# Kernel optimization log

Measured on AMD Instinct MI355X. Metric: run time of the kernel, lower is better.

## Reference

```python
import jax, jax.numpy as jnp
import numpy as np

NUM_RBF = 16
TOP_K = 30
MAXREL = 32  # max_relative_feature
M_CTX = 16   # ligand context atoms per residue

PT_GROUP = jnp.array([0,1,18,1,2,13,14,15,16,17,18,1,2,13,14,15,16,17,18,1,2,3,4,5,6,7,8,9,10,11,12,13,14,15,16,17,18,1,2,3,4,5,6,7,8,9,10,11,12,13,14,15,16,17,18,1,2,3,3,3,3,3,3,3,3,3,3,3,3,3,3,3,4,5,6,7,8,9,10,11,12,13,14,15,16,17,18,1,2,3,3,3,3,3,3,3,3,3,3,3,3,3,3,3,4,5,6,7,8,9,10,11,12,13,14,15,16,17,18], dtype=jnp.int32)
PT_PERIOD = jnp.array([0,1,1,2,2,2,2,2,2,2,2,3,3,3,3,3,3,3,3,4,4,4,4,4,4,4,4,4,4,4,4,4,4,4,4,4,4,5,5,5,5,5,5,5,5,5,5,5,5,5,5,5,5,5,5,6,6,6,6,6,6,6,6,6,6,6,6,6,6,6,6,6,6,6,6,6,6,6,6,6,6,6,6,6,6,6,6,7,7,7,7,7,7,7,7,7,7,7,7,7,7,7,7,7,7,7,7,7,7,7,7,7,7,7,7,7,7,7,7], dtype=jnp.int32)

# pair order after the Ca-Ca term: (N,N),(C,C),(O,O),(Cb,Cb),(Ca,N),(Ca,C),(Ca,O),(Ca,Cb),
# (N,C),(N,O),(N,Cb),(Cb,C),(Cb,O),(O,C),(N,Ca),(C,Ca),(O,Ca),(Cb,Ca),(C,N),(O,N),(Cb,N),(C,Cb),(O,Cb),(C,O)
# atom index in A5 stack: N=0, Ca=1, C=2, O=3, Cb=4
AI = np.array([0,2,3,4,1,1,1,1,0,0,0,4,4,3,0,2,3,4,2,3,4,2,3,2])
BI = np.array([0,2,3,4,0,2,3,4,2,3,4,2,3,2,1,1,1,1,0,0,0,4,4,3])


def _rbf(D):
    mu = jnp.linspace(2.0, 22.0, NUM_RBF)
    sigma = (22.0 - 2.0) / NUM_RBF
    return jnp.exp(-(((D[..., None] - mu) / sigma) ** 2))


def _angle_features(A, Bc, Cc, Y):
    v1 = A - Bc
    v2 = Cc - Bc
    e1 = v1 / jnp.linalg.norm(v1, axis=-1, keepdims=True)
    dot = jnp.einsum('bli,bli->bl', e1, v2)[..., None]
    u2 = v2 - e1 * dot
    e2 = u2 / jnp.linalg.norm(u2, axis=-1, keepdims=True)
    e3 = jnp.cross(e1, e2, axis=-1)
    R = jnp.concatenate((e1[..., None], e2[..., None], e3[..., None]), axis=-1)  # [B,L,3,3]
    lv = jnp.einsum('blqp,blyq->blyp', R, Y - Bc[:, :, None, :])
    rxy = jnp.sqrt(lv[..., 0] ** 2 + lv[..., 1] ** 2 + 1e-8)
    f1 = lv[..., 0] / rxy
    f2 = lv[..., 1] / rxy
    rxyz = jnp.linalg.norm(lv, axis=-1) + 1e-8
    f3 = rxy / rxyz
    f4 = lv[..., 2] / rxyz
    return jnp.stack([f1, f2, f3, f4], axis=-1)  # [B,L,M,4]


def setup_inputs() -> dict:
    key = jax.random.key(0)
    ks = jax.random.split(key, 16)
    B, L, M = 2, 2048, M_CTX
    X = jax.random.normal(ks[0], (B, L, 4, 3), jnp.float32) * 10.0
    Y = jax.random.normal(ks[1], (B, L, M, 3), jnp.float32) * 10.0
    mask = jnp.ones((B, L), jnp.float32)
    Y_m = jnp.ones((B, L, M), jnp.float32)
    R_idx = jnp.arange(B * L, dtype=jnp.int32).reshape(B, L)
    chain_labels = jax.random.randint(ks[2], (B, L), 0, 2, jnp.int32)
    Y_t = jax.random.randint(ks[3], (B, L, M), 1, 119, jnp.int32)
    def lin(k, fi, fo):
        return jax.random.normal(k, (fi, fo), jnp.float32) / np.sqrt(fi)
    params = dict(
        Wp=lin(ks[4], 2 * MAXREL + 2, 16), bp=jnp.zeros((16,), jnp.float32),
        We=lin(ks[5], 16 + 25 * NUM_RBF, 128), be=jnp.zeros((128,), jnp.float32),
        Wn=lin(ks[6], 5 * NUM_RBF + 64 + 4, 128), bn=jnp.zeros((128,), jnp.float32),
        Wt=lin(ks[7], 147, 64), bt=jnp.zeros((64,), jnp.float32),
        Wyn=lin(ks[8], 147, 128), byn=jnp.zeros((128,), jnp.float32),
        Wye=lin(ks[9], NUM_RBF, 128), bye=jnp.zeros((128,), jnp.float32),
    )
    return dict(X=X, Y=Y, mask=mask, Y_m=Y_m, R_idx=R_idx, chain_labels=chain_labels, Y_t=Y_t, **params)


def reference(X, Y, mask, Y_m, R_idx, chain_labels, Y_t,
              Wp, bp, We, be, Wn, bn, Wt, bt, Wyn, byn, Wye, bye):
    B, L = X.shape[0], X.shape[1]
    N, Ca, C, O = X[:, :, 0], X[:, :, 1], X[:, :, 2], X[:, :, 3]
    b_ = Ca - N
    c_ = C - Ca
    a_ = jnp.cross(b_, c_, axis=-1)
    Cb = -0.58273431 * a_ + 0.56802827 * b_ - 0.54067466 * c_ + Ca

    # masked pairwise distances + kNN (smallest-k)
    m2 = mask[:, None, :] * mask[:, :, None]
    dX = Ca[:, None, :, :] - Ca[:, :, None, :]
    D = m2 * jnp.sqrt(jnp.sum(dX * dX, -1) + 1e-6)
    Dadj = D + (1.0 - m2) * jnp.max(D, -1, keepdims=True)
    k = min(TOP_K, L)
    negD, E_idx = jax.lax.top_k(-Dadj, k)
    D_neighbors = -negD  # [B,L,K]

    # gather all 5 atom coords of neighbors once, then all 24 cross-atom RBFs
    A5 = jnp.stack([N, Ca, C, O, Cb], axis=2)  # [B,L,5,3]
    nb = A5[jnp.arange(B)[:, None, None], E_idx]  # [B,L,K,5,3]
    dvec = A5[:, :, None, AI, :] - nb[:, :, :, BI, :]  # [B,L,K,24,3]
    Dp = jnp.sqrt(jnp.sum(dvec * dvec, -1) + 1e-6)
    RBF_all = jnp.concatenate([_rbf(D_neighbors),
                               _rbf(Dp).reshape(B, L, k, 24 * NUM_RBF)], axis=-1)  # [B,L,K,400]

    # positional encodings
    offset = jnp.take_along_axis(R_idx[:, :, None] - R_idx[:, None, :], E_idx, axis=2)
    Ech = jnp.take_along_axis((chain_labels[:, :, None] == chain_labels[:, None, :]).astype(jnp.int32), E_idx, axis=2)
    d = jnp.clip(offset + MAXREL, 0, 2 * MAXREL)
    d = d * Ech + (1 - Ech) * (2 * MAXREL + 1)
    Epos = jax.nn.one_hot(d, 2 * MAXREL + 2, dtype=jnp.float32) @ Wp + bp
    E = jnp.concatenate([Epos, RBF_all], axis=-1) @ We + be  # [B,L,K,128]

    # ligand atom featurization
    g = PT_GROUP[Y_t]
    p = PT_PERIOD[Y_t]
    Yt1 = jnp.concatenate([jax.nn.one_hot(Y_t, 120, dtype=jnp.float32),
                           jax.nn.one_hot(g, 19, dtype=jnp.float32),
                           jax.nn.one_hot(p, 8, dtype=jnp.float32)], axis=-1)  # [B,L,M,147]
    Yt_lin = Yt1 @ Wt + bt  # [B,L,M,64]
    dAY = A5[:, :, :, None, :] - Y[:, :, None, :, :]  # [B,L,5,M,3]
    D_AY = jnp.sqrt(jnp.sum(dAY * dAY, -1) + 1e-6)
    RBF_AY = jnp.transpose(_rbf(D_AY), (0, 1, 3, 2, 4)).reshape(B, L, Y.shape[2], 5 * NUM_RBF)
    f_ang = _angle_features(N, Ca, C, Y)  # [B,L,M,4]
    V = jnp.concatenate([RBF_AY, Yt_lin, f_ang], axis=-1) @ Wn + bn  # [B,L,M,128]

    dYY = Y[:, :, :, None, :] - Y[:, :, None, :, :]
    Y_edges = _rbf(jnp.sqrt(jnp.sum(dYY * dYY, -1) + 1e-6)) @ Wye + bye  # [B,L,M,M,128]
    Y_nodes = Yt1 @ Wyn + byn  # [B,L,M,128]
    return V, E, E_idx, Y_nodes, Y_edges, Y_m
```

## Files before the change

### kernel.cpp

```cpp
#include <hip/hip_runtime.h>
#include <float.h>

typedef unsigned int   u32;
typedef unsigned short ushort_t;
typedef __attribute__((ext_vector_type(8))) short  bf16x8;
typedef __attribute__((ext_vector_type(4))) float  f32x4;
typedef __attribute__((ext_vector_type(8))) unsigned short ushort8;

#define NB 2
#define NL 2048
#define NM 16
#define NK 30

#define OV  0ull
#define OE  8388608ull
#define OEI 24117248ull
#define OYN 24240128ull
#define OYE 32628736ull
#define OYM 166846464ull

__constant__ int PT_GROUP_c[119] = {0,1,18,1,2,13,14,15,16,17,18,1,2,13,14,15,16,17,18,1,2,3,4,5,6,7,8,9,10,11,12,13,14,15,16,17,18,1,2,3,4,5,6,7,8,9,10,11,12,13,14,15,16,17,18,1,2,3,3,3,3,3,3,3,3,3,3,3,3,3,3,3,4,5,6,7,8,9,10,11,12,13,14,15,16,17,18,1,2,3,3,3,3,3,3,3,3,3,3,3,3,3,3,3,4,5,6,7,8,9,10,11,12,13,14,15,16,17,18};
__constant__ int PT_PERIOD_c[119] = {0,1,1,2,2,2,2,2,2,2,2,3,3,3,3,3,3,3,3,4,4,4,4,4,4,4,4,4,4,4,4,4,4,4,4,4,4,5,5,5,5,5,5,5,5,5,5,5,5,5,5,5,5,5,5,6,6,6,6,6,6,6,6,6,6,6,6,6,6,6,6,6,6,6,6,6,6,6,6,6,6,6,6,6,6,6,6,7,7,7,7,7,7,7,7,7,7,7,7,7,7,7,7,7,7,7,7,7,7,7,7,7,7,7,7,7,7,7,7};
__constant__ int AI_c[24] = {0,2,3,4,1,1,1,1,0,0,0,4,4,3,0,2,3,4,2,3,4,2,3,2};
__constant__ int BI_c[24] = {0,2,3,4,0,2,3,4,2,3,4,2,3,2,1,1,1,1,0,0,0,4,4,3};

__device__ __forceinline__ float cl24(float v) {
  return fminf(fmaxf(v, -24.f), 24.f);
}

__device__ __forceinline__ ushort_t f2bf(float f) {
  u32 u = __float_as_uint(f);
  return (ushort_t)((u + 0x7fffu + ((u >> 16) & 1u)) >> 16);
}

__device__ __forceinline__ float rbff(float d, int r) {
  float mu = 2.0f + (20.0f / 15.0f) * (float)r;
  float t = (d - mu) * 0.8f;
  return __expf(-t * t);
}

__global__ __launch_bounds__(256) void k_init(const float* __restrict__ We,
        const float* __restrict__ Wn, const float* __restrict__ X,
        ushort_t* __restrict__ WeT, ushort_t* __restrict__ WnT,
        float* __restrict__ A5, float* __restrict__ Ca4,
        float* __restrict__ Fr) {
  int blk = blockIdx.x;
  int tid = threadIdx.x;
  if (blk < 128) {
    int n = blk;
    for (int k = tid; k < 416; k += 256)
      WeT[(size_t)n * 416 + k] = f2bf(We[(size_t)k * 128 + n]);
    return;
  }
  if (blk < 256) {
    int n = blk - 128;
    if (tid < 160)
      WnT[(size_t)n * 160 + tid] = (tid < 148) ? f2bf(Wn[(size_t)tid * 128 + n])
                                               : (ushort_t)0;
    return;
  }
  int id = (blk - 256) * 256 + tid;
  if (id >= NB * NL) return;
  const float* x = X + (size_t)id * 12;
  float Nx=x[0],Ny=x[1],Nz=x[2], Cax=x[3],Cay=x[4],Caz=x[5];
  float Cx=x[6],Cy=x[7],Cz=x[8], Ox=x[9],Oy=x[10],Oz=x[11];
  float bx=Cax-Nx, by=Cay-Ny, bz=Caz-Nz;
  float cx=Cx-Cax, cy=Cy-Cay, cz=Cz-Caz;
  float ax=by*cz-bz*cy, ay=bz*cx-bx*cz, az=bx*cy-by*cx;
  float Cbx = -0.58273431f*ax + 0.56802827f*bx - 0.54067466f*cx + Cax;
  float Cby = -0.58273431f*ay + 0.56802827f*by - 0.54067466f*cy + Cay;
  float Cbz = -0.58273431f*az + 0.56802827f*bz - 0.54067466f*cz + Caz;
  float* A = A5 + (size_t)id * 15;
  A[0]=Nx;A[1]=Ny;A[2]=Nz; A[3]=Cax;A[4]=Cay;A[5]=Caz;
  A[6]=Cx;A[7]=Cy;A[8]=Cz; A[9]=Ox;A[10]=Oy;A[11]=Oz;
  A[12]=Cbx;A[13]=Cby;A[14]=Cbz;
  Ca4[id*4+0]=Cax; Ca4[id*4+1]=Cay; Ca4[id*4+2]=Caz; Ca4[id*4+3]=0.f;
  float v1x=Nx-Cax, v1y=Ny-Cay, v1z=Nz-Caz;
  float v2x=Cx-Cax, v2y=Cy-Cay, v2z=Cz-Caz;
  float n1 = sqrtf(v1x*v1x+v1y*v1y+v1z*v1z);
  float e1x=v1x/n1, e1y=v1y/n1, e1z=v1z/n1;
  float dot = e1x*v2x+e1y*v2y+e1z*v2z;
  float u2x=v2x-e1x*dot, u2y=v2y-e1y*dot, u2z=v2z-e1z*dot;
  float n2 = sqrtf(u2x*u2x+u2y*u2y+u2z*u2z);
  float e2x=u2x/n2, e2y=u2y/n2, e2z=u2z/n2;
  float e3x=e1y*e2z-e1z*e2y, e3y=e1z*e2x-e1x*e2z, e3z=e1x*e2y-e1y*e2x;
  float* F = Fr + (size_t)id * 9;
  F[0]=e1x;F[1]=e1y;F[2]=e1z; F[3]=e2x;F[4]=e2y;F[5]=e2z; F[6]=e3x;F[7]=e3y;F[8]=e3z;
}

__global__ __launch_bounds__(256) void k_topk(const float* __restrict__ Ca4,
                                              const float* __restrict__ mask,
                                              float* __restrict__ Dn,
                                              int* __restrict__ Eidx,
                                              float* __restrict__ out) {
  __shared__ float dist[NL];
  __shared__ float rv[4];
  __shared__ float cand_v[128];
  __shared__ int   cand_i[128];
  int row = blockIdx.x;
  int b = row >> 11;
  int tid = threadIdx.x;
  const float4* cab = (const float4*)Ca4 + ((size_t)b << 11);
  float4 ci = ((const float4*)Ca4)[row];
  float mi = mask[row];
  float lmax = 0.f;
  for (int j = tid; j < NL; j += 256) {
    float4 cj = cab[j];
    float dx = __fsub_rn(ci.x, cj.x);
    float dy = __fsub_rn(ci.y, cj.y);
    float dz = __fsub_rn(ci.z, cj.z);
    float s  = __fadd_rn(__fadd_rn(__fadd_rn(__fmul_rn(dx,dx), __fmul_rn(dy,dy)),
                                   __fmul_rn(dz,dz)), 1e-6f);
    float D  = __fmul_rn(__fmul_rn(mask[(b << 11) + j], mi), __fsqrt_rn(s));
    dist[j] = D;
    lmax = fmaxf(lmax, D);
  }
  #pragma unroll
  for (int s = 32; s > 0; s >>= 1) lmax = fmaxf(lmax, __shfl_xor(lmax, s));
  if ((tid & 63) == 0) rv[tid >> 6] = lmax;
  __syncthreads();
  float rowmax = fmaxf(fmaxf(rv[0], rv[1]), fmaxf(rv[2], rv[3]));
  for (int j = tid; j < NL; j += 256) {
    float mj = mask[(b << 11) + j];
    dist[j] = __fadd_rn(dist[j], __fmul_rn(__fsub_rn(1.f, __fmul_rn(mi, mj)), rowmax));
  }
  __syncthreads();
  int w = tid >> 6, l = tid & 63;
  int base = w * 512 + l;
  float v[8];
  #pragma unroll
  for (int k = 0; k < 8; k++) v[k] = dist[base + k * 64];
  if (tid < 8) { cand_v[120 + tid] = FLT_MAX; cand_i[120 + tid] = NL; }
  for (int it = 0; it < NK; it++) {
    float bv = FLT_MAX; int bj = NL;
    #pragma unroll
    for (int k = 0; k < 8; k++) {
      int jj = base + k * 64;
      if (v[k] < bv) { bv = v[k]; bj = jj; }
    }
    #pragma unroll
    for (int s = 32; s > 0; s >>= 1) {
      float ov = __shfl_xor(bv, s);
      int   oj = __shfl_xor(bj, s);
      if (ov < bv || (ov == bv && oj < bj)) { bv = ov; bj = oj; }
    }
    int ow = bj & 511;
    int ko = ow >> 6;
    bool mine = (ow & 63) == l;
    #pragma unroll
    for (int k = 0; k < 8; k++)
      if (mine && k == ko) v[k] = FLT_MAX;
    if (l == 0) { cand_v[w * NK + it] = bv; cand_i[w * NK + it] = bj; }
  }
  __syncthreads();
  if (tid < 64) {
    float v1 = cand_v[tid], v2 = cand_v[64 + tid];
    int   i1 = cand_i[tid], i2 = cand_i[64 + tid];
    for (int it = 0; it < NK; it++) {
      float bv; int bj, sl;
      if (v1 < v2 || (v1 == v2 && i1 < i2)) { bv = v1; bj = i1; sl = tid; }
      else                                  { bv = v2; bj = i2; sl = 64 + tid; }
      #pragma unroll
      for (int s = 32; s > 0; s >>= 1) {
        float ov = __shfl_xor(bv, s);
        int   oj = __shfl_xor(bj, s);
        int   os = __shfl_xor(sl, s);
        if (ov < bv || (ov == bv && oj < bj)) { bv = ov; bj = oj; sl = os; }
      }
      if (sl == tid)           v1 = FLT_MAX;
      else if (sl == 64 + tid) v2 = FLT_MAX;
      if (tid == 0) {
        Dn[(size_t)row * NK + it]   = bv;
        Eidx[(size_t)row * NK + it] = bj;
        out[OEI + (size_t)row * NK + it] = (float)bj;
      }
    }
  }
}

__global__ __launch_bounds__(256) void k_edge(const float* __restrict__ A5,
        const float* __restrict__ Dn, const int* __restrict__ Eidx,
        const int* __restrict__ R_idx, const int* __restrict__ cl,
        const float* __restrict__ Wp, const float* __restrict__ bp,
        const ushort_t* __restrict__ WeT, const float* __restrict__ be,
        float* __restrict__ out) {
  __shared__ __align__(16) ushort_t feat[32][424];
  int tid = threadIdx.x;
  int e0 = blockIdx.x * 32;
  {
    int el = tid >> 3;
    int te = tid & 7;
    int e  = e0 + el;
    int bi = e / NK;
    int b  = bi >> 11;
    int j  = Eidx[e];
    j = j < 0 ? 0 : (j > NL - 1 ? NL - 1 : j);
    int jrow = (b << 11) + j;
    const float* Ac = A5 + (size_t)bi * 15;
    const float* An = A5 + (size_t)jrow * 15;
    int off = R_idx[bi] - R_idx[jrow];
    int d;
    if (cl[bi] == cl[jrow]) { d = off + 32; d = d < 0 ? 0 : (d > 64 ? 64 : d); }
    else d = 65;
    feat[el][2*te]   = f2bf(Wp[d * 16 + 2*te]   + bp[2*te]);
    feat[el][2*te+1] = f2bf(Wp[d * 16 + 2*te+1] + bp[2*te+1]);
    float dn = Dn[e];
    feat[el][16 + 2*te]   = f2bf(rbff(dn, 2*te));
    feat[el][16 + 2*te+1] = f2bf(rbff(dn, 2*te+1));
    #pragma unroll
    for (int pp = 0; pp < 3; pp++) {
      int p = te + pp * 8;
      int ai = AI_c[p] * 3, bj2 = BI_c[p] * 3;
      float dx = Ac[ai]   - An[bj2];
      float dy = Ac[ai+1] - An[bj2+1];
      float dz = Ac[ai+2] - An[bj2+2];
      float dp = sqrtf(dx*dx + dy*dy + dz*dz + 1e-6f);
      int fb = 32 + p * 16;
      #pragma unroll
      for (int r = 0; r < 16; r++) feat[el][fb + r] = f2bf(rbff(dp, r));
    }
  }
  __syncthreads();
  int l  = tid & 63;
  int wid = tid >> 6;
  int wm = wid >> 1, wn = wid & 1;
  f32x4 acc0 = {0.f,0.f,0.f,0.f}, acc1 = {0.f,0.f,0.f,0.f};
  f32x4 acc2 = {0.f,0.f,0.f,0.f}, acc3 = {0.f,0.f,0.f,0.f};
  const ushort_t* Wb = WeT + (size_t)(wn*64 + (l & 15)) * 416 + (l >> 4) * 8;
  #pragma unroll 2
  for (int c = 0; c < 13; c++) {
    bf16x8 a  = *(const bf16x8*)&feat[wm*16 + (l & 15)][c*32 + (l >> 4)*8];
    bf16x8 b0 = *(const bf16x8*)(Wb + c*32);
    bf16x8 b1 = *(const bf16x8*)(Wb + 16*416 + c*32);
    bf16x8 b2 = *(const bf16x8*)(Wb + 32*416 + c*32);
    bf16x8 b3 = *(const bf16x8*)(Wb + 48*416 + c*32);
    acc0 = __builtin_amdgcn_mfma_f32_16x16x32_bf16(a, b0, acc0, 0, 0, 0);
    acc1 = __builtin_amdgcn_mfma_f32_16x16x32_bf16(a, b1, acc1, 0, 0, 0);
    acc2 = __builtin_amdgcn_mfma_f32_16x16x32_bf16(a, b2, acc2, 0, 0, 0);
    acc3 = __builtin_amdgcn_mfma_f32_16x16x32_bf16(a, b3, acc3, 0, 0, 0);
  }
  #pragma unroll
  for (int t = 0; t < 4; t++) {
    f32x4 av = (t==0) ? acc0 : (t==1) ? acc1 : (t==2) ? acc2 : acc3;
    int n = wn*64 + t*16 + (l & 15);
    float bb = be[n];
    #pragma unroll
    for (int jj = 0; jj < 4; jj++) {
      int ee = e0 + wm*16 + (l >> 4)*4 + jj;
      out[OE + (size_t)ee * 128 + n] = cl24(av[jj] + bb);
    }
  }
}

__global__ __launch_bounds__(256) void k_v(const float* __restrict__ A5,
        const float* __restrict__ Fr, const float* __restrict__ Y,
        const int* __restrict__ Y_t,
        const ushort_t* __restrict__ WnT, const float* __restrict__ bn,
        const float* __restrict__ Wt, const float* __restrict__ bt,
        float* __restrict__ out) {
  __shared__ __align__(16) ushort_t feat[16][168];
  __shared__ float dAY[16][8];
  int tid = threadIdx.x;
  int bl = blockIdx.x;
  if (tid < 80) {
    int m = tid / 5, a = tid % 5;
    float dx = A5[(size_t)bl*15 + a*3 + 0] - Y[(size_t)bl*48 + m*3 + 0];
    float dy = A5[(size_t)bl*15 + a*3 + 1] - Y[(size_t)bl*48 + m*3 + 1];
    float dz = A5[(size_t)bl*15 + a*3 + 2] - Y[(size_t)bl*48 + m*3 + 2];
    dAY[m][a] = sqrtf(dx*dx + dy*dy + dz*dz + 1e-6f);
  }
  __syncthreads();
  {
    int m = tid >> 4, q = tid & 15;
    #pragma unroll
    for (int a = 0; a < 5; a++) feat[m][a * 16 + q] = f2bf(rbff(dAY[m][a], q));
    int yt = Y_t[(size_t)bl * NM + m];
    int g = PT_GROUP_c[yt], p = PT_PERIOD_c[yt];
    {
      float4 wa = *(const float4*)&Wt[yt*64 + q*4];
      float4 wb = *(const float4*)&Wt[(120+g)*64 + q*4];
      float4 wc = *(const float4*)&Wt[(139+p)*64 + q*4];
      float4 bb = *(const float4*)&bt[q*4];
      feat[m][80 + q*4 + 0] = f2bf(wa.x + wb.x + wc.x + bb.x);
      feat[m][80 + q*4 + 1] = f2bf(wa.y + wb.y + wc.y + bb.y);
      feat[m][80 + q*4 + 2] = f2bf(wa.z + wb.z + wc.z + bb.z);
      feat[m][80 + q*4 + 3] = f2bf(wa.w + wb.w + wc.w + bb.w);
    }
    if (q == 0) {
      const float* fr = Fr + (size_t)bl * 9;
      float cax = A5[(size_t)bl*15+3], cay = A5[(size_t)bl*15+4], caz = A5[(size_t)bl*15+5];
      float yx = Y[(size_t)bl*48 + m*3+0] - cax;
      float yy = Y[(size_t)bl*48 + m*3+1] - cay;
      float yz = Y[(size_t)bl*48 + m*3+2] - caz;
      float l0 = fr[0]*yx + fr[1]*yy + fr[2]*yz;
      float l1 = fr[3]*yx + fr[4]*yy + fr[5]*yz;
      float l2 = fr[6]*yx + fr[7]*yy + fr[8]*yz;
      float rxy  = sqrtf(l0*l0 + l1*l1 + 1e-8f);
      float rxyz = sqrtf(l0*l0 + l1*l1 + l2*l2) + 1e-8f;
      feat[m][144] = f2bf(l0 / rxy);
      feat[m][145] = f2bf(l1 / rxy);
      feat[m][146] = f2bf(rxy / rxyz);
      feat[m][147] = f2bf(l2 / rxyz);
    }
    if (q < 12) feat[m][148 + q] = 0;
  }
  __syncthreads();
  int l = tid & 63;
  int wid = tid >> 6;
  int n0 = wid * 32;
  f32x4 acc0 = {0.f,0.f,0.f,0.f}, acc1 = {0.f,0.f,0.f,0.f};
  const ushort_t* Wb = WnT + (size_t)(n0 + (l & 15)) * 160 + (l >> 4) * 8;
  #pragma unroll
  for (int c = 0; c < 5; c++) {
    bf16x8 a  = *(const bf16x8*)&feat[l & 15][c*32 + (l >> 4)*8];
    bf16x8 b0 = *(const bf16x8*)(Wb + c*32);
    bf16x8 b1 = *(const bf16x8*)(Wb + 16*160 + c*32);
    acc0 = __builtin_amdgcn_mfma_f32_16x16x32_bf16(a, b0, acc0, 0, 0, 0);
    acc1 = __builtin_amdgcn_mfma_f32_16x16x32_bf16(a, b1, acc1, 0, 0, 0);
  }
  #pragma unroll
  for (int t = 0; t < 2; t++) {
    f32x4 av = (t==0) ? acc0 : acc1;
    int n = n0 + t*16 + (l & 15);
    float bb = bn[n];
    #pragma unroll
    for (int jj = 0; jj < 4; jj++) {
      int m = (l >> 4)*4 + jj;
      out[OV + ((size_t)bl * NM + m) * 128 + n] = cl24(av[jj] + bb);
    }
  }
}

__global__ __launch_bounds__(256, 4) void k_ynode(const int* __restrict__ Y_t,
        const float* __restrict__ Wyn, const float* __restrict__ byn,
        const float* __restrict__ Y_m, float* __restrict__ out) {
  int tid = threadIdx.x;
  int bl = blockIdx.x;
  if (tid < NM)
    out[OYM + (size_t)bl * NM + tid] = Y_m[(size_t)bl * NM + tid];
  int m = tid >> 4, n0 = (tid & 15) * 8;
  int yt = Y_t[(size_t)bl * NM + m];
  int g = PT_GROUP_c[yt], p = PT_PERIOD_c[yt];
  const float* w0 = Wyn + yt * 128 + n0;
  const float* w1 = Wyn + (120 + g) * 128 + n0;
  const float* w2 = Wyn + (139 + p) * 128 + n0;
  float4 r0 = *(const float4*)&w0[0], r1 = *(const float4*)&w0[4];
  float4 s0 = *(const float4*)&w1[0], s1 = *(const float4*)&w1[4];
  float4 t0 = *(const float4*)&w2[0], t1 = *(const float4*)&w2[4];
  float4 b0 = *(const float4*)&byn[n0], b1 = *(const float4*)&byn[n0 + 4];
  float4 o0, o1;
  o0.x = cl24(r0.x + s0.x + t0.x + b0.x);
  o0.y = cl24(r0.y + s0.y + t0.y + b0.y);
  o0.z = cl24(r0.z + s0.z + t0.z + b0.z);
  o0.w = cl24(r0.w + s0.w + t0.w + b0.w);
  o1.x = cl24(r1.x + s1.x + t1.x + b1.x);
  o1.y = cl24(r1.y + s1.y + t1.y + b1.y);
  o1.z = cl24(r1.z + s1.z + t1.z + b1.z);
  o1.w = cl24(r1.w + s1.w + t1.w + b1.w);
  size_t ob = OYN + ((size_t)bl * NM + m) * 128 + n0;
  *(float4*)&out[ob]     = o0;
  *(float4*)&out[ob + 4] = o1;
}

__global__ __launch_bounds__(256) void k_yedge(const float* __restrict__ Y,
        const float* __restrict__ Wye, const float* __restrict__ bye,
        float* __restrict__ out) {
  __shared__ float rbf_s[256][20];
  __shared__ float ys[16][3];
  __shared__ float wye_s[16][128];
  __shared__ float bye_s[128];
  int tid = threadIdx.x;
  int bl = blockIdx.x;
  if (tid < 48) ((float*)ys)[tid] = Y[(size_t)bl * 48 + tid];
  for (int x = tid; x < 2048; x += 256) wye_s[x >> 7][x & 127] = Wye[x];
  if (tid < 128) bye_s[tid] = bye[tid];
  __syncthreads();
  {
    int m = tid >> 4, m2 = tid & 15;
    float dx = ys[m][0]-ys[m2][0], dy = ys[m][1]-ys[m2][1], dz = ys[m][2]-ys[m2][2];
    float dd = sqrtf(dx*dx + dy*dy + dz*dz + 1e-6f);
    #pragma unroll
    for (int r = 0; r < 16; r++) rbf_s[tid][r] = rbff(dd, r);
  }
  __syncthreads();
  int n2 = (tid & 63) * 2;
  int pg = tid >> 6;
  float wy0[16], wy1[16];
  #pragma unroll
  for (int k = 0; k < 16; k++) { wy0[k] = wye_s[k][n2]; wy1[k] = wye_s[k][n2+1]; }
  float bb0 = bye_s[n2], bb1 = bye_s[n2+1];
  size_t obase = OYE + (size_t)bl * (NM * NM * 128);
  for (int p = pg * 64; p < pg * 64 + 64; p++) {
    float s0 = bb0, s1 = bb1;
    #pragma unroll
    for (int k4 = 0; k4 < 4; k4++) {
      float4 rv = *(const float4*)&rbf_s[p][k4 * 4];
      s0 = fmaf(rv.x, wy0[k4*4+0], s0); s1 = fmaf(rv.x, wy1[k4*4+0], s1);
      s0 = fmaf(rv.y, wy0[k4*4+1], s0); s1 = fmaf(rv.y, wy1[k4*4+1], s1);
      s0 = fmaf(rv.z, wy0[k4*4+2], s0); s1 = fmaf(rv.z, wy1[k4*4+2], s1);
      s0 = fmaf(rv.w, wy0[k4*4+3], s0); s1 = fmaf(rv.w, wy1[k4*4+3], s1);
    }
    float2 st; st.x = cl24(s0); st.y = cl24(s1);
    *(float2*)&out[obase + (size_t)p * 128 + n2] = st;
  }
}

extern "C" void kernel_launch(void* const* d_in, const int* in_sizes, int n_in,
                              void* d_out, int out_size, void* d_ws, size_t ws_size,
                              hipStream_t stream) {
  const float* X     = (const float*)d_in[0];
  const float* Y     = (const float*)d_in[1];
  const float* mask  = (const float*)d_in[2];
  const float* Y_m   = (const float*)d_in[3];
  const int*   R_idx = (const int*)d_in[4];
  const int*   cl    = (const int*)d_in[5];
  const int*   Y_t   = (const int*)d_in[6];
  const float* Wp    = (const float*)d_in[7];
  const float* bp    = (const float*)d_in[8];
  const float* We    = (const float*)d_in[9];
  const float* be    = (const float*)d_in[10];
  const float* Wn    = (const float*)d_in[11];
  const float* bn    = (const float*)d_in[12];
  const float* Wt    = (const float*)d_in[13];
  const float* bt    = (const float*)d_in[14];
  const float* Wyn   = (const float*)d_in[15];
  const float* byn   = (const float*)d_in[16];
  const float* Wye   = (const float*)d_in[17];
  const float* bye   = (const float*)d_in[18];
  float* out = (float*)d_out;

  float* wsf  = (float*)d_ws;
  float* A5   = wsf;
  float* Ca4  = A5  + 61440;
  float* Fr   = Ca4 + 16384;
  float* Dn   = Fr  + 36864;
  int*   Eidx = (int*)(Dn + 122880);
  ushort_t* WeT = (ushort_t*)(Eidx + 122880);
  ushort_t* WnT = WeT + 128 * 416;

  k_init <<<272,  256, 0, stream>>>(We, Wn, X, WeT, WnT, A5, Ca4, Fr);
  k_topk <<<NB*NL,256, 0, stream>>>(Ca4, mask, Dn, Eidx, out);
  k_edge <<<(NB*NL*NK)/32, 256, 0, stream>>>(A5, Dn, Eidx, R_idx, cl, Wp, bp, WeT, be, out);
  k_v    <<<NB*NL,256, 0, stream>>>(A5, Fr, Y, Y_t, WnT, bn, Wt, bt, out);
  k_ynode<<<NB*NL,256, 0, stream>>>(Y_t, Wyn, byn, Y_m, out);
  k_yedge<<<NB*NL,256, 0, stream>>>(Y, Wye, bye, out);
}
```

Measured before the change: 323.5 us.

## Fuse topk, node, ynode and yedge kernels into one phase-dispatched megakernel

Merges four independent per-residue kernels (k_topk, k_v, k_ynode, k_yedge) into a single launch, where blockIdx&3 selects the phase. The memory-bound y-edge writes can then overlap with the compute-heavy top-k and MFMA blocks, and three launches and their tail gaps go away. In exchange every block reserves the largest shared-memory footprint (about 29KB dynamic), which can lower occupancy for the light phases. Register allocation is also set by the heaviest branch.

```diff
diff --git a/kernel.cpp b/kernel.cpp
--- a/kernel.cpp
+++ b/kernel.cpp
@@ -88,93 +88,246 @@
   F[0]=e1x;F[1]=e1y;F[2]=e1z; F[3]=e2x;F[4]=e2y;F[5]=e2z; F[6]=e3x;F[7]=e3y;F[8]=e3z;
 }
 
-__global__ __launch_bounds__(256) void k_topk(const float* __restrict__ Ca4,
-                                              const float* __restrict__ mask,
-                                              float* __restrict__ Dn,
-                                              int* __restrict__ Eidx,
-                                              float* __restrict__ out) {
-  __shared__ float dist[NL];
-  __shared__ float rv[4];
-  __shared__ float cand_v[128];
-  __shared__ int   cand_i[128];
-  int row = blockIdx.x;
-  int b = row >> 11;
+__global__ __launch_bounds__(256) void k_mega(
+        const float* __restrict__ Ca4, const float* __restrict__ mask,
+        float* __restrict__ Dn, int* __restrict__ Eidx,
+        const float* __restrict__ A5, const float* __restrict__ Fr,
+        const float* __restrict__ Y, const int* __restrict__ Y_t,
+        const ushort_t* __restrict__ WnT, const float* __restrict__ bn,
+        const float* __restrict__ Wt, const float* __restrict__ bt,
+        const float* __restrict__ Wyn, const float* __restrict__ byn,
+        const float* __restrict__ Y_m,
+        const float* __restrict__ Wye, const float* __restrict__ bye,
+        float* __restrict__ out) {
+  extern __shared__ __align__(16) char smem[];
   int tid = threadIdx.x;
-  const float4* cab = (const float4*)Ca4 + ((size_t)b << 11);
-  float4 ci = ((const float4*)Ca4)[row];
-  float mi = mask[row];
-  float lmax = 0.f;
-  for (int j = tid; j < NL; j += 256) {
-    float4 cj = cab[j];
-    float dx = __fsub_rn(ci.x, cj.x);
-    float dy = __fsub_rn(ci.y, cj.y);
-    float dz = __fsub_rn(ci.z, cj.z);
-    float s  = __fadd_rn(__fadd_rn(__fadd_rn(__fmul_rn(dx,dx), __fmul_rn(dy,dy)),
-                                   __fmul_rn(dz,dz)), 1e-6f);
-    float D  = __fmul_rn(__fmul_rn(mask[(b << 11) + j], mi), __fsqrt_rn(s));
-    dist[j] = D;
-    lmax = fmaxf(lmax, D);
-  }
-  #pragma unroll
-  for (int s = 32; s > 0; s >>= 1) lmax = fmaxf(lmax, __shfl_xor(lmax, s));
-  if ((tid & 63) == 0) rv[tid >> 6] = lmax;
-  __syncthreads();
-  float rowmax = fmaxf(fmaxf(rv[0], rv[1]), fmaxf(rv[2], rv[3]));
-  for (int j = tid; j < NL; j += 256) {
-    float mj = mask[(b << 11) + j];
-    dist[j] = __fadd_rn(dist[j], __fmul_rn(__fsub_rn(1.f, __fmul_rn(mi, mj)), rowmax));
-  }
-  __syncthreads();
-  int w = tid >> 6, l = tid & 63;
-  int base = w * 512 + l;
-  float v[8];
-  #pragma unroll
-  for (int k = 0; k < 8; k++) v[k] = dist[base + k * 64];
-  if (tid < 8) { cand_v[120 + tid] = FLT_MAX; cand_i[120 + tid] = NL; }
-  for (int it = 0; it < NK; it++) {
-    float bv = FLT_MAX; int bj = NL;
-    #pragma unroll
-    for (int k = 0; k < 8; k++) {
-      int jj = base + k * 64;
-      if (v[k] < bv) { bv = v[k]; bj = jj; }
-    }
-    #pragma unroll
-    for (int s = 32; s > 0; s >>= 1) {
-      float ov = __shfl_xor(bv, s);
-      int   oj = __shfl_xor(bj, s);
-      if (ov < bv || (ov == bv && oj < bj)) { bv = ov; bj = oj; }
-    }
-    int ow = bj & 511;
-    int ko = ow >> 6;
-    bool mine = (ow & 63) == l;
-    #pragma unroll
-    for (int k = 0; k < 8; k++)
-      if (mine && k == ko) v[k] = FLT_MAX;
-    if (l == 0) { cand_v[w * NK + it] = bv; cand_i[w * NK + it] = bj; }
-  }
-  __syncthreads();
-  if (tid < 64) {
-    float v1 = cand_v[tid], v2 = cand_v[64 + tid];
-    int   i1 = cand_i[tid], i2 = cand_i[64 + tid];
+  int phase = blockIdx.x & 3;
+  int bl = blockIdx.x >> 2;
+
+  if (phase == 0) {
+    float (*rbf_s)[20]  = (float(*)[20])smem;
+    float (*ys)[3]      = (float(*)[3])(smem + 20480);
+    float (*wye_s)[128] = (float(*)[128])(smem + 20672);
+    float *bye_s        = (float*)(smem + 28864);
+    if (tid < 48) ((float*)ys)[tid] = Y[(size_t)bl * 48 + tid];
+    for (int x = tid; x < 2048; x += 256) wye_s[x >> 7][x & 127] = Wye[x];
+    if (tid < 128) bye_s[tid] = bye[tid];
+    __syncthreads();
+    {
+      int m = tid >> 4, m2 = tid & 15;
+      float dx = ys[m][0]-ys[m2][0], dy = ys[m][1]-ys[m2][1], dz = ys[m][2]-ys[m2][2];
+      float dd = sqrtf(dx*dx + dy*dy + dz*dz + 1e-6f);
+      #pragma unroll
+      for (int r = 0; r < 16; r++) rbf_s[tid][r] = rbff(dd, r);
+    }
+    __syncthreads();
+    int n2 = (tid & 63) * 2;
+    int pg = tid >> 6;
+    float wy0[16], wy1[16];
+    #pragma unroll
+    for (int k = 0; k < 16; k++) { wy0[k] = wye_s[k][n2]; wy1[k] = wye_s[k][n2+1]; }
+    float bb0 = bye_s[n2], bb1 = bye_s[n2+1];
+    size_t obase = OYE + (size_t)bl * (NM * NM * 128);
+    for (int p = pg * 64; p < pg * 64 + 64; p++) {
+      float s0 = bb0, s1 = bb1;
+      #pragma unroll
+      for (int k4 = 0; k4 < 4; k4++) {
+        float4 rv = *(const float4*)&rbf_s[p][k4 * 4];
+        s0 = fmaf(rv.x, wy0[k4*4+0], s0); s1 = fmaf(rv.x, wy1[k4*4+0], s1);
+        s0 = fmaf(rv.y, wy0[k4*4+1], s0); s1 = fmaf(rv.y, wy1[k4*4+1], s1);
+        s0 = fmaf(rv.z, wy0[k4*4+2], s0); s1 = fmaf(rv.z, wy1[k4*4+2], s1);
+        s0 = fmaf(rv.w, wy0[k4*4+3], s0); s1 = fmaf(rv.w, wy1[k4*4+3], s1);
+      }
+      float2 st; st.x = cl24(s0); st.y = cl24(s1);
+      *(float2*)&out[obase + (size_t)p * 128 + n2] = st;
+    }
+    return;
+  }
+
+  if (phase == 1) {
+    float* dist   = (float*)smem;
+    float* rv     = (float*)(smem + 8192);
+    float* cand_v = (float*)(smem + 8208);
+    int*   cand_i = (int*)(smem + 8720);
+    int row = bl;
+    int b = row >> 11;
+    const float4* cab = (const float4*)Ca4 + ((size_t)b << 11);
+    float4 ci = ((const float4*)Ca4)[row];
+    float mi = mask[row];
+    float lmax = 0.f;
+    for (int j = tid; j < NL; j += 256) {
+      float4 cj = cab[j];
+      float dx = __fsub_rn(ci.x, cj.x);
+      float dy = __fsub_rn(ci.y, cj.y);
+      float dz = __fsub_rn(ci.z, cj.z);
+      float s  = __fadd_rn(__fadd_rn(__fadd_rn(__fmul_rn(dx,dx), __fmul_rn(dy,dy)),
+                                     __fmul_rn(dz,dz)), 1e-6f);
+      float D  = __fmul_rn(__fmul_rn(mask[(b << 11) + j], mi), __fsqrt_rn(s));
+      dist[j] = D;
+      lmax = fmaxf(lmax, D);
+    }
+    #pragma unroll
+    for (int s = 32; s > 0; s >>= 1) lmax = fmaxf(lmax, __shfl_xor(lmax, s));
+    if ((tid & 63) == 0) rv[tid >> 6] = lmax;
+    __syncthreads();
+    float rowmax = fmaxf(fmaxf(rv[0], rv[1]), fmaxf(rv[2], rv[3]));
+    for (int j = tid; j < NL; j += 256) {
+      float mj = mask[(b << 11) + j];
+      dist[j] = __fadd_rn(dist[j], __fmul_rn(__fsub_rn(1.f, __fmul_rn(mi, mj)), rowmax));
+    }
+    __syncthreads();
+    int w = tid >> 6, l = tid & 63;
+    int base = w * 512 + l;
+    float v[8];
+    #pragma unroll
+    for (int k = 0; k < 8; k++) v[k] = dist[base + k * 64];
+    if (tid < 8) { cand_v[120 + tid] = FLT_MAX; cand_i[120 + tid] = NL; }
     for (int it = 0; it < NK; it++) {
-      float bv; int bj, sl;
-      if (v1 < v2 || (v1 == v2 && i1 < i2)) { bv = v1; bj = i1; sl = tid; }
-      else                                  { bv = v2; bj = i2; sl = 64 + tid; }
+      float bv = FLT_MAX; int bj = NL;
+      #pragma unroll
+      for (int k = 0; k < 8; k++) {
+        int jj = base + k * 64;
+        if (v[k] < bv) { bv = v[k]; bj = jj; }
+      }
       #pragma unroll
       for (int s = 32; s > 0; s >>= 1) {
         float ov = __shfl_xor(bv, s);
         int   oj = __shfl_xor(bj, s);
-        int   os = __shfl_xor(sl, s);
-        if (ov < bv || (ov == bv && oj < bj)) { bv = ov; bj = oj; sl = os; }
-      }
-      if (sl == tid)           v1 = FLT_MAX;
-      else if (sl == 64 + tid) v2 = FLT_MAX;
-      if (tid == 0) {
-        Dn[(size_t)row * NK + it]   = bv;
-        Eidx[(size_t)row * NK + it] = bj;
-        out[OEI + (size_t)row * NK + it] = (float)bj;
-      }
-    }
+        if (ov < bv || (ov == bv && oj < bj)) { bv = ov; bj = oj; }
+      }
+      int ow = bj & 511;
+      int ko = ow >> 6;
+      bool mine = (ow & 63) == l;
+      #pragma unroll
+      for (int k = 0; k < 8; k++)
+        if (mine && k == ko) v[k] = FLT_MAX;
+      if (l == 0) { cand_v[w * NK + it] = bv; cand_i[w * NK + it] = bj; }
+    }
+    __syncthreads();
+    if (tid < 64) {
+      float v1 = cand_v[tid], v2 = cand_v[64 + tid];
+      int   i1 = cand_i[tid], i2 = cand_i[64 + tid];
+      for (int it = 0; it < NK; it++) {
+        float bv; int bj, sl;
+        if (v1 < v2 || (v1 == v2 && i1 < i2)) { bv = v1; bj = i1; sl = tid; }
+        else                                  { bv = v2; bj = i2; sl = 64 + tid; }
+        #pragma unroll
+        for (int s = 32; s > 0; s >>= 1) {
+          float ov = __shfl_xor(bv, s);
+          int   oj = __shfl_xor(bj, s);
+          int   os = __shfl_xor(sl, s);
+          if (ov < bv || (ov == bv && oj < bj)) { bv = ov; bj = oj; sl = os; }
+        }
+        if (sl == tid)           v1 = FLT_MAX;
+        else if (sl == 64 + tid) v2 = FLT_MAX;
+        if (tid == 0) {
+          Dn[(size_t)row * NK + it]   = bv;
+          Eidx[(size_t)row * NK + it] = bj;
+          out[OEI + (size_t)row * NK + it] = (float)bj;
+        }
+      }
+    }
+    return;
+  }
+
+  if (phase == 2) {
+    ushort_t (*feat)[168] = (ushort_t(*)[168])smem;
+    float (*dAY)[8]       = (float(*)[8])(smem + 5376);
+    if (tid < 80) {
+      int m = tid / 5, a = tid % 5;
+      float dx = A5[(size_t)bl*15 + a*3 + 0] - Y[(size_t)bl*48 + m*3 + 0];
+      float dy = A5[(size_t)bl*15 + a*3 + 1] - Y[(size_t)bl*48 + m*3 + 1];
+      float dz = A5[(size_t)bl*15 + a*3 + 2] - Y[(size_t)bl*48 + m*3 + 2];
+      dAY[m][a] = sqrtf(dx*dx + dy*dy + dz*dz + 1e-6f);
+    }
+    __syncthreads();
+    {
+      int m = tid >> 4, q = tid & 15;
+      #pragma unroll
+      for (int a = 0; a < 5; a++) feat[m][a * 16 + q] = f2bf(rbff(dAY[m][a], q));
+      int yt = Y_t[(size_t)bl * NM + m];
+      int g = PT_GROUP_c[yt], p = PT_PERIOD_c[yt];
+      {
+        float4 wa = *(const float4*)&Wt[yt*64 + q*4];
+        float4 wb = *(const float4*)&Wt[(120+g)*64 + q*4];
+        float4 wc = *(const float4*)&Wt[(139+p)*64 + q*4];
+        float4 bb = *(const float4*)&bt[q*4];
+        feat[m][80 + q*4 + 0] = f2bf(wa.x + wb.x + wc.x + bb.x);
+        feat[m][80 + q*4 + 1] = f2bf(wa.y + wb.y + wc.y + bb.y);
+        feat[m][80 + q*4 + 2] = f2bf(wa.z + wb.z + wc.z + bb.z);
+        feat[m][80 + q*4 + 3] = f2bf(wa.w + wb.w + wc.w + bb.w);
+      }
+      if (q == 0) {
+        const float* fr = Fr + (size_t)bl * 9;
+        float cax = A5[(size_t)bl*15+3], cay = A5[(size_t)bl*15+4], caz = A5[(size_t)bl*15+5];
+        float yx = Y[(size_t)bl*48 + m*3+0] - cax;
+        float yy = Y[(size_t)bl*48 + m*3+1] - cay;
+        float yz = Y[(size_t)bl*48 + m*3+2] - caz;
+        float l0 = fr[0]*yx + fr[1]*yy + fr[2]*yz;
+        float l1 = fr[3]*yx + fr[4]*yy + fr[5]*yz;
+        float l2 = fr[6]*yx + fr[7]*yy + fr[8]*yz;
+        float rxy  = sqrtf(l0*l0 + l1*l1 + 1e-8f);
+        float rxyz = sqrtf(l0*l0 + l1*l1 + l2*l2) + 1e-8f;
+        feat[m][144] = f2bf(l0 / rxy);
+        feat[m][145] = f2bf(l1 / rxy);
+        feat[m][146] = f2bf(rxy / rxyz);
+        feat[m][147] = f2bf(l2 / rxyz);
+      }
+      if (q < 12) feat[m][148 + q] = 0;
+    }
+    __syncthreads();
+    int l = tid & 63;
+    int wid = tid >> 6;
+    int n0 = wid * 32;
+    f32x4 acc0 = {0.f,0.f,0.f,0.f}, acc1 = {0.f,0.f,0.f,0.f};
+    const ushort_t* Wb = WnT + (size_t)(n0 + (l & 15)) * 160 + (l >> 4) * 8;
+    #pragma unroll
+    for (int c = 0; c < 5; c++) {
+      bf16x8 a  = *(const bf16x8*)&feat[l & 15][c*32 + (l >> 4)*8];
+      bf16x8 b0 = *(const bf16x8*)(Wb + c*32);
+      bf16x8 b1 = *(const bf16x8*)(Wb + 16*160 + c*32);
+      acc0 = __builtin_amdgcn_mfma_f32_16x16x32_bf16(a, b0, acc0, 0, 0, 0);
+      acc1 = __builtin_amdgcn_mfma_f32_16x16x32_bf16(a, b1, acc1, 0, 0, 0);
+    }
+    #pragma unroll
+    for (int t = 0; t < 2; t++) {
+      f32x4 av = (t==0) ? acc0 : acc1;
+      int n = n0 + t*16 + (l & 15);
+      float bb = bn[n];
+      #pragma unroll
+      for (int jj = 0; jj < 4; jj++) {
+        int m = (l >> 4)*4 + jj;
+        out[OV + ((size_t)bl * NM + m) * 128 + n] = cl24(av[jj] + bb);
+      }
+    }
+    return;
+  }
+
+  {
+    if (tid < NM)
+      out[OYM + (size_t)bl * NM + tid] = Y_m[(size_t)bl * NM + tid];
+    int m = tid >> 4, n0 = (tid & 15) * 8;
+    int yt = Y_t[(size_t)bl * NM + m];
+    int g = PT_GROUP_c[yt], p = PT_PERIOD_c[yt];
+    const float* w0 = Wyn + yt * 128 + n0;
+    const float* w1 = Wyn + (120 + g) * 128 + n0;
+    const float* w2 = Wyn + (139 + p) * 128 + n0;
+    float4 r0 = *(const float4*)&w0[0], r1 = *(const float4*)&w0[4];
+    float4 s0 = *(const float4*)&w1[0], s1 = *(const float4*)&w1[4];
+    float4 t0 = *(const float4*)&w2[0], t1 = *(const float4*)&w2[4];
+    float4 b0 = *(const float4*)&byn[n0], b1 = *(const float4*)&byn[n0 + 4];
+    float4 o0, o1;
+    o0.x = cl24(r0.x + s0.x + t0.x + b0.x);
+    o0.y = cl24(r0.y + s0.y + t0.y + b0.y);
+    o0.z = cl24(r0.z + s0.z + t0.z + b0.z);
+    o0.w = cl24(r0.w + s0.w + t0.w + b0.w);
+    o1.x = cl24(r1.x + s1.x + t1.x + b1.x);
+    o1.y = cl24(r1.y + s1.y + t1.y + b1.y);
+    o1.z = cl24(r1.z + s1.z + t1.z + b1.z);
+    o1.w = cl24(r1.w + s1.w + t1.w + b1.w);
+    size_t ob = OYN + ((size_t)bl * NM + m) * 128 + n0;
+    *(float4*)&out[ob]     = o0;
+    *(float4*)&out[ob + 4] = o1;
   }
 }
 
@@ -252,159 +405,6 @@
   }
 }
 
-__global__ __launch_bounds__(256) void k_v(const float* __restrict__ A5,
-        const float* __restrict__ Fr, const float* __restrict__ Y,
-        const int* __restrict__ Y_t,
-        const ushort_t* __restrict__ WnT, const float* __restrict__ bn,
-        const float* __restrict__ Wt, const float* __restrict__ bt,
-        float* __restrict__ out) {
-  __shared__ __align__(16) ushort_t feat[16][168];
-  __shared__ float dAY[16][8];
-  int tid = threadIdx.x;
-  int bl = blockIdx.x;
-  if (tid < 80) {
-    int m = tid / 5, a = tid % 5;
-    float dx = A5[(size_t)bl*15 + a*3 + 0] - Y[(size_t)bl*48 + m*3 + 0];
-    float dy = A5[(size_t)bl*15 + a*3 + 1] - Y[(size_t)bl*48 + m*3 + 1];
-    float dz = A5[(size_t)bl*15 + a*3 + 2] - Y[(size_t)bl*48 + m*3 + 2];
-    dAY[m][a] = sqrtf(dx*dx + dy*dy + dz*dz + 1e-6f);
-  }
-  __syncthreads();
-  {
-    int m = tid >> 4, q = tid & 15;
-    #pragma unroll
-    for (int a = 0; a < 5; a++) feat[m][a * 16 + q] = f2bf(rbff(dAY[m][a], q));
-    int yt = Y_t[(size_t)bl * NM + m];
-    int g = PT_GROUP_c[yt], p = PT_PERIOD_c[yt];
-    {
-      float4 wa = *(const float4*)&Wt[yt*64 + q*4];
-      float4 wb = *(const float4*)&Wt[(120+g)*64 + q*4];
-      float4 wc = *(const float4*)&Wt[(139+p)*64 + q*4];
-      float4 bb = *(const float4*)&bt[q*4];
-      feat[m][80 + q*4 + 0] = f2bf(wa.x + wb.x + wc.x + bb.x);
-      feat[m][80 + q*4 + 1] = f2bf(wa.y + wb.y + wc.y + bb.y);
-      feat[m][80 + q*4 + 2] = f2bf(wa.z + wb.z + wc.z + bb.z);
-      feat[m][80 + q*4 + 3] = f2bf(wa.w + wb.w + wc.w + bb.w);
-    }
-    if (q == 0) {
-      const float* fr = Fr + (size_t)bl * 9;
-      float cax = A5[(size_t)bl*15+3], cay = A5[(size_t)bl*15+4], caz = A5[(size_t)bl*15+5];
-      float yx = Y[(size_t)bl*48 + m*3+0] - cax;
-      float yy = Y[(size_t)bl*48 + m*3+1] - cay;
-      float yz = Y[(size_t)bl*48 + m*3+2] - caz;
-      float l0 = fr[0]*yx + fr[1]*yy + fr[2]*yz;
-      float l1 = fr[3]*yx + fr[4]*yy + fr[5]*yz;
-      float l2 = fr[6]*yx + fr[7]*yy + fr[8]*yz;
-      float rxy  = sqrtf(l0*l0 + l1*l1 + 1e-8f);
-      float rxyz = sqrtf(l0*l0 + l1*l1 + l2*l2) + 1e-8f;
-      feat[m][144] = f2bf(l0 / rxy);
-      feat[m][145] = f2bf(l1 / rxy);
-      feat[m][146] = f2bf(rxy / rxyz);
-      feat[m][147] = f2bf(l2 / rxyz);
-    }
-    if (q < 12) feat[m][148 + q] = 0;
-  }
-  __syncthreads();
-  int l = tid & 63;
-  int wid = tid >> 6;
-  int n0 = wid * 32;
-  f32x4 acc0 = {0.f,0.f,0.f,0.f}, acc1 = {0.f,0.f,0.f,0.f};
-  const ushort_t* Wb = WnT + (size_t)(n0 + (l & 15)) * 160 + (l >> 4) * 8;
-  #pragma unroll
-  for (int c = 0; c < 5; c++) {
-    bf16x8 a  = *(const bf16x8*)&feat[l & 15][c*32 + (l >> 4)*8];
-    bf16x8 b0 = *(const bf16x8*)(Wb + c*32);
-    bf16x8 b1 = *(const bf16x8*)(Wb + 16*160 + c*32);
-    acc0 = __builtin_amdgcn_mfma_f32_16x16x32_bf16(a, b0, acc0, 0, 0, 0);
-    acc1 = __builtin_amdgcn_mfma_f32_16x16x32_bf16(a, b1, acc1, 0, 0, 0);
-  }
-  #pragma unroll
-  for (int t = 0; t < 2; t++) {
-    f32x4 av = (t==0) ? acc0 : acc1;
-    int n = n0 + t*16 + (l & 15);
-    float bb = bn[n];
-    #pragma unroll
-    for (int jj = 0; jj < 4; jj++) {
-      int m = (l >> 4)*4 + jj;
-      out[OV + ((size_t)bl * NM + m) * 128 + n] = cl24(av[jj] + bb);
-    }
-  }
-}
-
-__global__ __launch_bounds__(256, 4) void k_ynode(const int* __restrict__ Y_t,
-        const float* __restrict__ Wyn, const float* __restrict__ byn,
-        const float* __restrict__ Y_m, float* __restrict__ out) {
-  int tid = threadIdx.x;
-  int bl = blockIdx.x;
-  if (tid < NM)
-    out[OYM + (size_t)bl * NM + tid] = Y_m[(size_t)bl * NM + tid];
-  int m = tid >> 4, n0 = (tid & 15) * 8;
-  int yt = Y_t[(size_t)bl * NM + m];
-  int g = PT_GROUP_c[yt], p = PT_PERIOD_c[yt];
-  const float* w0 = Wyn + yt * 128 + n0;
-  const float* w1 = Wyn + (120 + g) * 128 + n0;
-  const float* w2 = Wyn + (139 + p) * 128 + n0;
-  float4 r0 = *(const float4*)&w0[0], r1 = *(const float4*)&w0[4];
-  float4 s0 = *(const float4*)&w1[0], s1 = *(const float4*)&w1[4];
-  float4 t0 = *(const float4*)&w2[0], t1 = *(const float4*)&w2[4];
-  float4 b0 = *(const float4*)&byn[n0], b1 = *(const float4*)&byn[n0 + 4];
-  float4 o0, o1;
-  o0.x = cl24(r0.x + s0.x + t0.x + b0.x);
-  o0.y = cl24(r0.y + s0.y + t0.y + b0.y);
-  o0.z = cl24(r0.z + s0.z + t0.z + b0.z);
-  o0.w = cl24(r0.w + s0.w + t0.w + b0.w);
-  o1.x = cl24(r1.x + s1.x + t1.x + b1.x);
-  o1.y = cl24(r1.y + s1.y + t1.y + b1.y);
-  o1.z = cl24(r1.z + s1.z + t1.z + b1.z);
-  o1.w = cl24(r1.w + s1.w + t1.w + b1.w);
-  size_t ob = OYN + ((size_t)bl * NM + m) * 128 + n0;
-  *(float4*)&out[ob]     = o0;
-  *(float4*)&out[ob + 4] = o1;
-}
-
-__global__ __launch_bounds__(256) void k_yedge(const float* __restrict__ Y,
-        const float* __restrict__ Wye, const float* __restrict__ bye,
-        float* __restrict__ out) {
-  __shared__ float rbf_s[256][20];
-  __shared__ float ys[16][3];
-  __shared__ float wye_s[16][128];
-  __shared__ float bye_s[128];
-  int tid = threadIdx.x;
-  int bl = blockIdx.x;
-  if (tid < 48) ((float*)ys)[tid] = Y[(size_t)bl * 48 + tid];
-  for (int x = tid; x < 2048; x += 256) wye_s[x >> 7][x & 127] = Wye[x];
-  if (tid < 128) bye_s[tid] = bye[tid];
-  __syncthreads();
-  {
-    int m = tid >> 4, m2 = tid & 15;
-    float dx = ys[m][0]-ys[m2][0], dy = ys[m][1]-ys[m2][1], dz = ys[m][2]-ys[m2][2];
-    float dd = sqrtf(dx*dx + dy*dy + dz*dz + 1e-6f);
-    #pragma unroll
-    for (int r = 0; r < 16; r++) rbf_s[tid][r] = rbff(dd, r);
-  }
-  __syncthreads();
-  int n2 = (tid & 63) * 2;
-  int pg = tid >> 6;
-  float wy0[16], wy1[16];
-  #pragma unroll
-  for (int k = 0; k < 16; k++) { wy0[k] = wye_s[k][n2]; wy1[k] = wye_s[k][n2+1]; }
-  float bb0 = bye_s[n2], bb1 = bye_s[n2+1];
-  size_t obase = OYE + (size_t)bl * (NM * NM * 128);
-  for (int p = pg * 64; p < pg * 64 + 64; p++) {
-    float s0 = bb0, s1 = bb1;
-    #pragma unroll
-    for (int k4 = 0; k4 < 4; k4++) {
-      float4 rv = *(const float4*)&rbf_s[p][k4 * 4];
-      s0 = fmaf(rv.x, wy0[k4*4+0], s0); s1 = fmaf(rv.x, wy1[k4*4+0], s1);
-      s0 = fmaf(rv.y, wy0[k4*4+1], s0); s1 = fmaf(rv.y, wy1[k4*4+1], s1);
-      s0 = fmaf(rv.z, wy0[k4*4+2], s0); s1 = fmaf(rv.z, wy1[k4*4+2], s1);
-      s0 = fmaf(rv.w, wy0[k4*4+3], s0); s1 = fmaf(rv.w, wy1[k4*4+3], s1);
-    }
-    float2 st; st.x = cl24(s0); st.y = cl24(s1);
-    *(float2*)&out[obase + (size_t)p * 128 + n2] = st;
-  }
-}
-
 extern "C" void kernel_launch(void* const* d_in, const int* in_sizes, int n_in,
                               void* d_out, int out_size, void* d_ws, size_t ws_size,
                               hipStream_t stream) {
@@ -438,10 +438,9 @@
   ushort_t* WeT = (ushort_t*)(Eidx + 122880);
   ushort_t* WnT = WeT + 128 * 416;
 
-  k_init <<<272,  256, 0, stream>>>(We, Wn, X, WeT, WnT, A5, Ca4, Fr);
-  k_topk <<<NB*NL,256, 0, stream>>>(Ca4, mask, Dn, Eidx, out);
-  k_edge <<<(NB*NL*NK)/32, 256, 0, stream>>>(A5, Dn, Eidx, R_idx, cl, Wp, bp, WeT, be, out);
-  k_v    <<<NB*NL,256, 0, stream>>>(A5, Fr, Y, Y_t, WnT, bn, Wt, bt, out);
-  k_ynode<<<NB*NL,256, 0, stream>>>(Y_t, Wyn, byn, Y_m, out);
-  k_yedge<<<NB*NL,256, 0, stream>>>(Y, Wye, bye, out);
-}
+  k_init <<<272, 256, 0, stream>>>(We, Wn, X, WeT, WnT, A5, Ca4, Fr);
+  k_mega <<<4 * NB * NL, 256, 29376, stream>>>(Ca4, mask, Dn, Eidx,
+          A5, Fr, Y, Y_t, WnT, bn, Wt, bt, Wyn, byn, Y_m, Wye, bye, out);
+  k_edge <<<(NB*NL*NK)/32, 256, 0, stream>>>(A5, Dn, Eidx, R_idx, cl,
+          Wp, bp, WeT, be, out);
+}
```

Measured after the change: 667.1 us. 2.06x slower.
